# Kernel tuning notes

Hardware: AMD Instinct MI355X
Metric: run time of the kernel (lower is better)

## Reference

```python
import jax, jax.numpy as jnp
import numpy as np

WS = 7        # window_size
NH = 12       # num_heads
HD = 32       # head_dim
DIM = 384     # dim
N = WS * WS   # tokens per window


def _cpb_rel_coords():
    # log-spaced relative coords, (N, N, 2)
    c = np.stack(np.meshgrid(np.arange(WS), np.arange(WS), indexing='ij'))  # (2, ws, ws)
    cf = c.reshape(2, -1)                       # (2, N)
    rel = cf[:, :, None] - cf[:, None, :]       # (2, N, N)
    rel = rel.transpose(1, 2, 0).astype(np.float32)  # (N, N, 2)
    return np.sign(rel) * np.log1p(np.abs(rel))


def setup_inputs() -> dict:
    key = jax.random.key(0)
    ks = jax.random.split(key, 6)
    B_ = 2048
    x = jax.random.normal(ks[0], (B_, N, DIM), jnp.float32)
    mask = jnp.zeros((64, N, N), jnp.float32)  # shifted-window mask (0 / -100 pattern); zeros here
    qkv_w = jax.random.normal(ks[1], (3 * DIM, DIM), jnp.float32) * 0.02
    qkv_b = jnp.zeros((3 * DIM,), jnp.float32)
    tau = jnp.ones((NH,), jnp.float32)
    cpb_w1 = jax.random.normal(ks[2], (64, 2), jnp.float32) * 0.02
    cpb_b1 = jnp.zeros((64,), jnp.float32)
    cpb_w2 = jax.random.normal(ks[3], (NH, 64), jnp.float32) * 0.02
    cpb_b2 = jnp.zeros((NH,), jnp.float32)
    proj_w = jax.random.normal(ks[4], (DIM, DIM), jnp.float32) * 0.02
    proj_b = jnp.zeros((DIM,), jnp.float32)
    return {"x": x, "mask": mask, "qkv_w": qkv_w, "qkv_b": qkv_b, "tau": tau,
            "cpb_w1": cpb_w1, "cpb_b1": cpb_b1, "cpb_w2": cpb_w2, "cpb_b2": cpb_b2,
            "proj_w": proj_w, "proj_b": proj_b}


def reference(x, mask, qkv_w, qkv_b, tau, cpb_w1, cpb_b1, cpb_w2, cpb_b2, proj_w, proj_b):
    B_, Nt, C = x.shape
    qkv = x @ qkv_w.T + qkv_b                         # (B_, N, 3*C)
    qkv = qkv.reshape(B_, Nt, 3, NH, HD).transpose(2, 0, 3, 1, 4)  # (3, B_, H, N, hd)
    q, k, v = qkv[0], qkv[1], qkv[2]
    # cosine attention: L2-normalize q, k (F.normalize eps=1e-12)
    q = q / jnp.maximum(jnp.linalg.norm(q, axis=-1, keepdims=True), 1e-12)
    k = k / jnp.maximum(jnp.linalg.norm(k, axis=-1, keepdims=True), 1e-12)
    attn = jnp.einsum('bhnd,bhmd->bhnm', q, k)        # (B_, H, N, N)
    attn = attn / jnp.maximum(tau, 0.01)[None, :, None, None]
    # log-CPB bias
    rel = jnp.asarray(_cpb_rel_coords())              # (N, N, 2)
    cpb = jax.nn.relu(rel @ cpb_w1.T + cpb_b1) @ cpb_w2.T + cpb_b2  # (N, N, H)
    attn = attn + cpb.transpose(2, 0, 1)[None]        # broadcast over B_
    # shifted-window mask
    nW = mask.shape[0]
    B = B_ // nW
    attn = (attn.reshape(B, nW, NH, Nt, Nt) + mask[None, :, None]).reshape(B_, NH, Nt, Nt)
    attn = jax.nn.softmax(attn, axis=-1)
    y = jnp.einsum('bhnm,bhmd->bnhd', attn, v).reshape(B_, Nt, C)
    return y @ proj_w.T + proj_b
```

## Files before the change

### kernel.cpp

```cpp
#include <hip/hip_runtime.h>


typedef float f32x4 __attribute__((ext_vector_type(4)));
typedef __bf16 bf16x8 __attribute__((ext_vector_type(8)));
typedef unsigned short u16;
typedef u16 u16x8 __attribute__((ext_vector_type(8)));
typedef u16 u16x4 __attribute__((ext_vector_type(4)));
typedef unsigned u32x4 __attribute__((ext_vector_type(4)));

__device__ __forceinline__ float b2f(unsigned u) {
  return __builtin_bit_cast(float, u << 16);
}
__device__ __forceinline__ u16 f2b(float f) {
  unsigned u = __builtin_bit_cast(unsigned, f);
  u += 0x7fffu + ((u >> 16) & 1u);
  return (u16)(u >> 16);
}
__device__ __forceinline__ unsigned pack2(float a, float b) {
  return (unsigned)f2b(a) | ((unsigned)f2b(b) << 16);
}

#define GLD16(gp, lp)                                        \
  __builtin_amdgcn_global_load_lds(                          \
      (const __attribute__((address_space(1))) void*)(gp),   \
      (__attribute__((address_space(3))) void*)(lp), 16, 0, 0)

__global__ __launch_bounds__(256) void k_cast(const float* __restrict__ in,
                                              u16* __restrict__ out, int n8) {
  int i = blockIdx.x * 256 + threadIdx.x;
  if (i >= n8) return;
  const float4* p = reinterpret_cast<const float4*>(in) + (size_t)i * 2;
  float4 a = p[0], b = p[1];
  u16x8 r;
  r[0] = f2b(a.x); r[1] = f2b(a.y); r[2] = f2b(a.z); r[3] = f2b(a.w);
  r[4] = f2b(b.x); r[5] = f2b(b.y); r[6] = f2b(b.z); r[7] = f2b(b.w);
  *(reinterpret_cast<u16x8*>(out) + i) = r;
}

__global__ __launch_bounds__(64) void k_cpb(const float* __restrict__ w1,
                                            const float* __restrict__ b1,
                                            const float* __restrict__ w2,
                                            const float* __restrict__ b2,
                                            float* __restrict__ cpb_t) {
  int p = blockIdx.x * 64 + threadIdx.x;
  if (p >= 49 * 49) return;
  int n = p / 49, m = p % 49;
  float d0 = (float)(n / 7 - m / 7);
  float d1 = (float)(n % 7 - m % 7);
  float a0 = log1pf(fabsf(d0)); a0 = (d0 < 0.f) ? -a0 : a0;
  float a1 = log1pf(fabsf(d1)); a1 = (d1 < 0.f) ? -a1 : a1;
  float acc[12];
#pragma unroll
  for (int h = 0; h < 12; ++h) acc[h] = b2[h];
  for (int j = 0; j < 64; ++j) {
    float hj = fmaxf(a0 * w1[2 * j] + a1 * w1[2 * j + 1] + b1[j], 0.f);
#pragma unroll
    for (int h = 0; h < 12; ++h) acc[h] += hj * w2[h * 64 + j];
  }
#pragma unroll
  for (int h = 0; h < 12; ++h) cpb_t[h * 2401 + p] = acc[h];
}

__global__ __launch_bounds__(256) void k_comb(const float* __restrict__ cpb_t,
                                              const float* __restrict__ mask,
                                              float* __restrict__ comb) {
  const int wh = blockIdx.x;
  const int h = wh >> 6, w = wh & 63;
  const float* c = cpb_t + h * 2401;
  const float* m = mask + (size_t)w * 2401;
  float* o = comb + (size_t)wh * 2548;
  for (int p = threadIdx.x; p < 2548; p += 256) {
    int n = p / 52, mc = p % 52;
    float v = (mc < 49) ? c[n * 49 + mc] + m[n * 49 + mc] : 0.f;
    o[p] = v;
  }
}

template <bool OUT_F32>
__global__ __launch_bounds__(256) void k_gemm_bt(
    const u16* __restrict__ A, const u16* __restrict__ W,
    const float* __restrict__ bias, void* __restrict__ Cv,
    int M, int N, int K) {
  (void)M;
  __shared__ __align__(16) u16 sA[2][4096];
  __shared__ __align__(16) u16 sB[2][4096];
  const int tid = threadIdx.x;
  const int cpx = (int)(gridDim.x >> 3);
  int bid = (int)blockIdx.x;
  bid = (bid & 7) * cpx + (bid >> 3);
  const int nt = N >> 7;
  const int m0 = (bid / nt) << 7;
  const int n0 = (bid % nt) << 7;
  const int srow = tid >> 2;
  const int scs = (((tid & 3) ^ ((srow >> 1) & 3)) << 3);
  const u16* ga0 = A + (size_t)(m0 + srow) * K + scs;
  const u16* ga1 = ga0 + (size_t)64 * K;
  const u16* gw0 = W + (size_t)(n0 + srow) * K + scs;
  const u16* gw1 = gw0 + (size_t)64 * K;
  const int KT = K >> 5;

#define STAGE(buf, kk)                              \
  do {                                              \
    GLD16(ga0 + (kk), &sA[buf][tid * 8]);           \
    GLD16(ga1 + (kk), &sA[buf][2048 + tid * 8]);    \
    GLD16(gw0 + (kk), &sB[buf][tid * 8]);           \
    GLD16(gw1 + (kk), &sB[buf][2048 + tid * 8]);    \
  } while (0)

  STAGE(0, 0);

  const f32x4 z4 = {0.f, 0.f, 0.f, 0.f};
  f32x4 acc[4][4];
#pragma unroll
  for (int i = 0; i < 4; ++i)
#pragma unroll
    for (int j = 0; j < 4; ++j) acc[i][j] = z4;

  const int l = tid & 63, w = tid >> 6;
  const int wm = (w >> 1) << 6, wn = (w & 1) << 6;
  const int lr = l & 15, lg = l >> 4;
  const int arow = wm + lr, brow = wn + lr;
  const int cg = ((lg ^ ((lr >> 1) & 3)) << 3);

  for (int t = 0; t < KT; ++t) {
    __syncthreads();
    if (t + 1 < KT) STAGE((t + 1) & 1, (t + 1) * 32);
    const u16* pa = sA[t & 1];
    const u16* pb = sB[t & 1];
    bf16x8 af[4], bfv[4];
#pragma unroll
    for (int mi = 0; mi < 4; ++mi)
      af[mi] = __builtin_bit_cast(bf16x8,
          *reinterpret_cast<const u16x8*>(pa + (arow + mi * 16) * 32 + cg));
#pragma unroll
    for (int ni = 0; ni < 4; ++ni)
      bfv[ni] = __builtin_bit_cast(bf16x8,
          *reinterpret_cast<const u16x8*>(pb + (brow + ni * 16) * 32 + cg));
#pragma unroll
    for (int mi = 0; mi < 4; ++mi)
#pragma unroll
      for (int ni = 0; ni < 4; ++ni)
        acc[mi][ni] = __builtin_amdgcn_mfma_f32_16x16x32_bf16(
            af[mi], bfv[ni], acc[mi][ni], 0, 0, 0);
  }
#undef STAGE

  float bv[4];
#pragma unroll
  for (int ni = 0; ni < 4; ++ni) bv[ni] = bias[n0 + wn + ni * 16 + lr];
#pragma unroll
  for (int mi = 0; mi < 4; ++mi)
#pragma unroll
    for (int r = 0; r < 4; ++r) {
      const size_t row = (size_t)(m0 + wm + mi * 16 + lg * 4 + r);
#pragma unroll
      for (int ni = 0; ni < 4; ++ni) {
        const int col = n0 + wn + ni * 16 + lr;
        float v = acc[mi][ni][r] + bv[ni];
        if (OUT_F32)
          reinterpret_cast<float*>(Cv)[row * N + col] = v;
        else
          reinterpret_cast<u16*>(Cv)[row * N + col] = f2b(v);
      }
    }
}

__global__ __launch_bounds__(64, 4) void k_attn(
    const u16* __restrict__ qkv, const float* __restrict__ tau,
    const float* __restrict__ comb, u16* __restrict__ y) {
  const int b = blockIdx.x, h = blockIdx.y;
  const int l = threadIdx.x;
  __shared__ __align__(16) u16 lk[64][40];
  __shared__ __align__(16) u16 lq[64][40];
  u16(*vt)[72] = reinterpret_cast<u16(*)[72]>(&lk[0][0]);

  const float tauh = fmaxf(tau[h], 0.01f);
  const bool valid = l < 49;
  u16x8 v8s[4];
  {
    const u16* base = qkv + ((size_t)b * 49 + (valid ? l : 0)) * 1152 + h * 32;
    float qv[32], kv[32];
#pragma unroll
    for (int c = 0; c < 4; ++c) {
      u16x8 q8 = {0, 0, 0, 0, 0, 0, 0, 0};
      u16x8 k8 = {0, 0, 0, 0, 0, 0, 0, 0};
      u16x8 v8 = {0, 0, 0, 0, 0, 0, 0, 0};
      if (valid) {
        q8 = *reinterpret_cast<const u16x8*>(base + c * 8);
        k8 = *reinterpret_cast<const u16x8*>(base + 384 + c * 8);
        v8 = *reinterpret_cast<const u16x8*>(base + 768 + c * 8);
      }
      v8s[c] = v8;
#pragma unroll
      for (int e = 0; e < 8; ++e) {
        qv[c * 8 + e] = b2f((unsigned)q8[e]);
        kv[c * 8 + e] = b2f((unsigned)k8[e]);
      }
    }
    float sq = 0.f, sk = 0.f;
#pragma unroll
    for (int j = 0; j < 32; ++j) { sq += qv[j] * qv[j]; sk += kv[j] * kv[j]; }
    const float qs = (1.f / fmaxf(sqrtf(sq), 1e-12f)) / tauh;
    const float ks = 1.f / fmaxf(sqrtf(sk), 1e-12f);
#pragma unroll
    for (int c = 0; c < 4; ++c) {
      u16x8 wq, wk;
#pragma unroll
      for (int e = 0; e < 8; ++e) {
        wq[e] = f2b(qv[c * 8 + e] * qs);
        wk[e] = f2b(kv[c * 8 + e] * ks);
      }
      *reinterpret_cast<u16x8*>(&lq[l][c * 8]) = wq;
      *reinterpret_cast<u16x8*>(&lk[l][c * 8]) = wk;
    }
  }
  __syncthreads();

  const int lr = l & 15, lg = l >> 4;
  bf16x8 kf[4];
#pragma unroll
  for (int mi = 0; mi < 4; ++mi)
    kf[mi] = __builtin_bit_cast(bf16x8,
        *reinterpret_cast<const u16x8*>(&lk[mi * 16 + lr][lg * 8]));
  __syncthreads();
#pragma unroll
  for (int c = 0; c < 4; ++c)
#pragma unroll
    for (int e = 0; e < 8; ++e) vt[c * 8 + e][l] = v8s[c][e];
  __syncthreads();
  bf16x8 vtf[2][2];
#pragma unroll
  for (int dd = 0; dd < 2; ++dd)
#pragma unroll
    for (int ks = 0; ks < 2; ++ks)
      vtf[dd][ks] = __builtin_bit_cast(bf16x8,
          *reinterpret_cast<const u16x8*>(&vt[dd * 16 + lr][ks * 32 + lg * 8]));

  const f32x4 z4 = {0.f, 0.f, 0.f, 0.f};
  const int src0 = lr + 16 * ((2 * lg) & 3);
  const int src1 = lr + 16 * ((2 * lg + 1) & 3);
  const bool hi5 = lg >= 2;
  const float* bbase = comb + (size_t)(h * 64 + (b & 63)) * 2548;

#pragma unroll
  for (int nj = 0; nj < 4; ++nj) {
    const bf16x8 qf = __builtin_bit_cast(bf16x8,
        *reinterpret_cast<const u16x8*>(&lq[nj * 16 + lr][lg * 8]));
    f32x4 s[4];
#pragma unroll
    for (int mi = 0; mi < 4; ++mi)
      s[mi] = __builtin_amdgcn_mfma_f32_16x16x32_bf16(kf[mi], qf, z4, 0, 0, 0);

    const int n = nj * 16 + lr;
    const float* bp = bbase + (size_t)(n < 49 ? n : 48) * 52 + lg * 4;
    f32x4 bia[4];
#pragma unroll
    for (int mi = 0; mi < 4; ++mi)
      bia[mi] = *reinterpret_cast<const f32x4*>(bp + mi * 16);

    float v[4][4];
#pragma unroll
    for (int mi = 0; mi < 3; ++mi)
#pragma unroll
      for (int r = 0; r < 4; ++r) v[mi][r] = s[mi][r] + bia[mi][r];
#pragma unroll
    for (int r = 0; r < 4; ++r) {
      float t = s[3][r] + bia[3][r];
      v[3][r] = (lg == 0 && r == 0) ? t : -1e30f;
    }

    float mx = v[0][0];
#pragma unroll
    for (int mi = 0; mi < 4; ++mi)
#pragma unroll
      for (int r = 0; r < 4; ++r) mx = fmaxf(mx, v[mi][r]);
    mx = fmaxf(mx, __shfl_xor(mx, 16));
    mx = fmaxf(mx, __shfl_xor(mx, 32));
    float sum = 0.f;
#pragma unroll
    for (int mi = 0; mi < 4; ++mi)
#pragma unroll
      for (int r = 0; r < 4; ++r) {
        v[mi][r] = __expf(v[mi][r] - mx);
        sum += v[mi][r];
      }
    sum += __shfl_xor(sum, 16);
    sum += __shfl_xor(sum, 32);
    const float rinv = __builtin_amdgcn_rcpf(sum);

    unsigned pk[4][2];
#pragma unroll
    for (int mi = 0; mi < 4; ++mi) {
      pk[mi][0] = pack2(v[mi][0] * rinv, v[mi][1] * rinv);
      pk[mi][1] = pack2(v[mi][2] * rinv, v[mi][3] * rinv);
    }
    bf16x8 pf[2];
#pragma unroll
    for (int ks = 0; ks < 2; ++ks) {
      unsigned a0 = (unsigned)__shfl((int)pk[2 * ks][0], src0);
      unsigned b0 = (unsigned)__shfl((int)pk[2 * ks + 1][0], src0);
      unsigned a1 = (unsigned)__shfl((int)pk[2 * ks][1], src0);
      unsigned b1 = (unsigned)__shfl((int)pk[2 * ks + 1][1], src0);
      unsigned a2 = (unsigned)__shfl((int)pk[2 * ks][0], src1);
      unsigned b2_ = (unsigned)__shfl((int)pk[2 * ks + 1][0], src1);
      unsigned a3 = (unsigned)__shfl((int)pk[2 * ks][1], src1);
      unsigned b3 = (unsigned)__shfl((int)pk[2 * ks + 1][1], src1);
      u32x4 ww = {hi5 ? b0 : a0, hi5 ? b1 : a1, hi5 ? b2_ : a2, hi5 ? b3 : a3};
      pf[ks] = __builtin_bit_cast(bf16x8, ww);
    }

    f32x4 o0 = __builtin_amdgcn_mfma_f32_16x16x32_bf16(vtf[0][0], pf[0], z4, 0, 0, 0);
    o0 = __builtin_amdgcn_mfma_f32_16x16x32_bf16(vtf[0][1], pf[1], o0, 0, 0, 0);
    f32x4 o1 = __builtin_amdgcn_mfma_f32_16x16x32_bf16(vtf[1][0], pf[0], z4, 0, 0, 0);
    o1 = __builtin_amdgcn_mfma_f32_16x16x32_bf16(vtf[1][1], pf[1], o1, 0, 0, 0);

    if (n < 49) {
      u16* dst = y + ((size_t)b * 49 + n) * 384 + h * 32 + lg * 4;
      u16x4 w0 = {f2b(o0[0]), f2b(o0[1]), f2b(o0[2]), f2b(o0[3])};
      u16x4 w1 = {f2b(o1[0]), f2b(o1[1]), f2b(o1[2]), f2b(o1[3])};
      *reinterpret_cast<u16x4*>(dst) = w0;
      *reinterpret_cast<u16x4*>(dst + 16) = w1;
    }
  }
}

extern "C" void kernel_launch(void* const* d_in, const int* in_sizes, int n_in,
                              void* d_out, int out_size, void* d_ws,
                              size_t ws_size, hipStream_t stream) {
  (void)in_sizes; (void)n_in; (void)out_size; (void)ws_size;
  const float* x      = (const float*)d_in[0];
  const float* mask   = (const float*)d_in[1];
  const float* qkv_w  = (const float*)d_in[2];
  const float* qkv_b  = (const float*)d_in[3];
  const float* tau    = (const float*)d_in[4];
  const float* cpb_w1 = (const float*)d_in[5];
  const float* cpb_b1 = (const float*)d_in[6];
  const float* cpb_w2 = (const float*)d_in[7];
  const float* cpb_b2 = (const float*)d_in[8];
  const float* proj_w = (const float*)d_in[9];
  const float* proj_b = (const float*)d_in[10];
  float* out = (float*)d_out;

  char* ws = (char*)d_ws;
  u16* x_bf     = (u16*)(ws);
  u16* qkvw_bf  = (u16*)(ws + 77070336);
  u16* projw_bf = (u16*)(ws + 77955072);
  float* cpb_t  = (float*)(ws + 78249984);
  u16* qkv_bf   = (u16*)(ws + 78365696);
  u16* y_bf     = (u16*)(ws + 309576704);
  float* comb   = (float*)(ws + 386647040);

  k_cast<<<dim3(18816), dim3(256), 0, stream>>>(x, x_bf, 4816896);
  k_cast<<<dim3(216), dim3(256), 0, stream>>>(qkv_w, qkvw_bf, 55296);
  k_cast<<<dim3(72), dim3(256), 0, stream>>>(proj_w, projw_bf, 18432);
  k_cpb<<<dim3(38), dim3(64), 0, stream>>>(cpb_w1, cpb_b1, cpb_w2, cpb_b2, cpb_t);
  k_comb<<<dim3(768), dim3(256), 0, stream>>>(cpb_t, mask, comb);

  k_gemm_bt<false><<<dim3(784 * 9), dim3(256), 0, stream>>>(
      x_bf, qkvw_bf, qkv_b, qkv_bf, 100352, 1152, 384);

  k_attn<<<dim3(2048, 12), dim3(64), 0, stream>>>(qkv_bf, tau, comb, y_bf);

  k_gemm_bt<true><<<dim3(784 * 3), dim3(256), 0, stream>>>(
      y_bf, projw_bf, proj_b, out, 100352, 384, 384);
}
```

Measured before the change: 423.5 us.

## Rewrite GEMM as 512-thread 256x128 tile with triple-buffered K=64 pipeline

```diff
diff --git a/kernel.cpp b/kernel.cpp
--- a/kernel.cpp
+++ b/kernel.cpp
@@ -24,6 +24,13 @@
   __builtin_amdgcn_global_load_lds(                          \
       (const __attribute__((address_space(1))) void*)(gp),   \
       (__attribute__((address_space(3))) void*)(lp), 16, 0, 0)
+
+#define BARF()                            \
+  do {                                    \
+    asm volatile("" ::: "memory");        \
+    __builtin_amdgcn_s_barrier();         \
+    asm volatile("" ::: "memory");        \
+  } while (0)
 
 __global__ __launch_bounds__(256) void k_cast(const float* __restrict__ in,
                                               u16* __restrict__ out, int n8) {
@@ -77,37 +84,41 @@
 }
 
 template <bool OUT_F32>
-__global__ __launch_bounds__(256) void k_gemm_bt(
+__global__ __launch_bounds__(512, 2) void k_gemm8(
     const u16* __restrict__ A, const u16* __restrict__ W,
-    const float* __restrict__ bias, void* __restrict__ Cv,
-    int M, int N, int K) {
-  (void)M;
-  __shared__ __align__(16) u16 sA[2][4096];
-  __shared__ __align__(16) u16 sB[2][4096];
+    const float* __restrict__ bias, void* __restrict__ Cv, int N) {
+  __shared__ __align__(16) u16 sA[3][16384];
+  __shared__ __align__(16) u16 sB[3][8192];
   const int tid = threadIdx.x;
   const int cpx = (int)(gridDim.x >> 3);
   int bid = (int)blockIdx.x;
   bid = (bid & 7) * cpx + (bid >> 3);
   const int nt = N >> 7;
-  const int m0 = (bid / nt) << 7;
+  const int m0 = (bid / nt) << 8;
   const int n0 = (bid % nt) << 7;
-  const int srow = tid >> 2;
-  const int scs = (((tid & 3) ^ ((srow >> 1) & 3)) << 3);
-  const u16* ga0 = A + (size_t)(m0 + srow) * K + scs;
-  const u16* ga1 = ga0 + (size_t)64 * K;
-  const u16* gw0 = W + (size_t)(n0 + srow) * K + scs;
-  const u16* gw1 = gw0 + (size_t)64 * K;
-  const int KT = K >> 5;
-
-#define STAGE(buf, kk)                              \
-  do {                                              \
-    GLD16(ga0 + (kk), &sA[buf][tid * 8]);           \
-    GLD16(ga1 + (kk), &sA[buf][2048 + tid * 8]);    \
-    GLD16(gw0 + (kk), &sB[buf][tid * 8]);           \
-    GLD16(gw1 + (kk), &sB[buf][2048 + tid * 8]);    \
-  } while (0)
-
-  STAGE(0, 0);
+
+  const int r0 = tid >> 3;
+  const int g = (((tid & 7) ^ (r0 & 7)) << 3);
+  const u16* pAg = A + (size_t)(m0 + r0) * 384 + g;
+  const u16* pBg = W + (size_t)(n0 + r0) * 384 + g;
+
+#define GA(buf, t, i) GLD16(pAg + (i) * 24576 + (t) * 64, &sA[buf][(i) * 4096 + tid * 8])
+#define GB(buf, t, i) GLD16(pBg + (i) * 24576 + (t) * 64, &sB[buf][(i) * 4096 + tid * 8])
+
+  GA(0, 0, 0); GA(0, 0, 1); GA(0, 0, 2); GA(0, 0, 3); GB(0, 0, 0); GB(0, 0, 1);
+  GA(1, 1, 0); GA(1, 1, 1); GA(1, 1, 2); GA(1, 1, 3); GB(1, 1, 0); GB(1, 1, 1);
+
+  const int l = tid & 63, w = tid >> 6;
+  const int wm = (w & 3) << 6, wn = (w >> 2) << 6;
+  const int lr = l & 15, lg = l >> 4;
+  const int ax = lr & 7;
+  const int sl0 = ((lg ^ ax) << 3), sl1 = (((4 | lg) ^ ax) << 3);
+  int aOff[4], bOff[4];
+#pragma unroll
+  for (int i = 0; i < 4; ++i) {
+    aOff[i] = (wm + i * 16 + lr) << 6;
+    bOff[i] = (wn + i * 16 + lr) << 6;
+  }
 
   const f32x4 z4 = {0.f, 0.f, 0.f, 0.f};
   f32x4 acc[4][4];
@@ -116,34 +127,61 @@
 #pragma unroll
     for (int j = 0; j < 4; ++j) acc[i][j] = z4;
 
-  const int l = tid & 63, w = tid >> 6;
-  const int wm = (w >> 1) << 6, wn = (w & 1) << 6;
-  const int lr = l & 15, lg = l >> 4;
-  const int arow = wm + lr, brow = wn + lr;
-  const int cg = ((lg ^ ((lr >> 1) & 3)) << 3);
-
-  for (int t = 0; t < KT; ++t) {
-    __syncthreads();
-    if (t + 1 < KT) STAGE((t + 1) & 1, (t + 1) * 32);
-    const u16* pa = sA[t & 1];
-    const u16* pb = sB[t & 1];
-    bf16x8 af[4], bfv[4];
+  asm volatile("s_waitcnt vmcnt(6)" ::: "memory");
+  __builtin_amdgcn_s_barrier();
+
+#pragma unroll
+  for (int t = 0; t < 6; ++t) {
+    const u16* pa = sA[t % 3];
+    const u16* pb = sB[t % 3];
+    const int nb = (t + 2) % 3;
+    bf16x8 af[4], bq[4];
 #pragma unroll
     for (int mi = 0; mi < 4; ++mi)
       af[mi] = __builtin_bit_cast(bf16x8,
-          *reinterpret_cast<const u16x8*>(pa + (arow + mi * 16) * 32 + cg));
+          *reinterpret_cast<const u16x8*>(pa + aOff[mi] + sl0));
 #pragma unroll
     for (int ni = 0; ni < 4; ++ni)
-      bfv[ni] = __builtin_bit_cast(bf16x8,
-          *reinterpret_cast<const u16x8*>(pb + (brow + ni * 16) * 32 + cg));
+      bq[ni] = __builtin_bit_cast(bf16x8,
+          *reinterpret_cast<const u16x8*>(pb + bOff[ni] + sl0));
+    if (t < 4) { GA(nb, t + 2, 0); GA(nb, t + 2, 1); GA(nb, t + 2, 2); }
+    BARF();
+    __builtin_amdgcn_s_setprio(1);
 #pragma unroll
     for (int mi = 0; mi < 4; ++mi)
 #pragma unroll
       for (int ni = 0; ni < 4; ++ni)
         acc[mi][ni] = __builtin_amdgcn_mfma_f32_16x16x32_bf16(
-            af[mi], bfv[ni], acc[mi][ni], 0, 0, 0);
-  }
-#undef STAGE
+            af[mi], bq[ni], acc[mi][ni], 0, 0, 0);
+    __builtin_amdgcn_s_setprio(0);
+    BARF();
+#pragma unroll
+    for (int mi = 0; mi < 4; ++mi)
+      af[mi] = __builtin_bit_cast(bf16x8,
+          *reinterpret_cast<const u16x8*>(pa + aOff[mi] + sl1));
+#pragma unroll
+    for (int ni = 0; ni < 4; ++ni)
+      bq[ni] = __builtin_bit_cast(bf16x8,
+          *reinterpret_cast<const u16x8*>(pb + bOff[ni] + sl1));
+    if (t < 4) { GA(nb, t + 2, 3); GB(nb, t + 2, 0); GB(nb, t + 2, 1); }
+    BARF();
+    __builtin_amdgcn_s_setprio(1);
+#pragma unroll
+    for (int mi = 0; mi < 4; ++mi)
+#pragma unroll
+      for (int ni = 0; ni < 4; ++ni)
+        acc[mi][ni] = __builtin_amdgcn_mfma_f32_16x16x32_bf16(
+            af[mi], bq[ni], acc[mi][ni], 0, 0, 0);
+    __builtin_amdgcn_s_setprio(0);
+    if (t < 4) {
+      asm volatile("s_waitcnt vmcnt(6)" ::: "memory");
+    } else if (t == 4) {
+      asm volatile("s_waitcnt vmcnt(0)" ::: "memory");
+    }
+    BARF();
+  }
+#undef GA
+#undef GB
 
   float bv[4];
 #pragma unroll
@@ -151,12 +189,12 @@
 #pragma unroll
   for (int mi = 0; mi < 4; ++mi)
 #pragma unroll
-    for (int r = 0; r < 4; ++r) {
-      const size_t row = (size_t)(m0 + wm + mi * 16 + lg * 4 + r);
+    for (int rr = 0; rr < 4; ++rr) {
+      const size_t row = (size_t)(m0 + wm + mi * 16 + lg * 4 + rr);
 #pragma unroll
       for (int ni = 0; ni < 4; ++ni) {
         const int col = n0 + wn + ni * 16 + lr;
-        float v = acc[mi][ni][r] + bv[ni];
+        float v = acc[mi][ni][rr] + bv[ni];
         if (OUT_F32)
           reinterpret_cast<float*>(Cv)[row * N + col] = v;
         else
@@ -356,11 +394,11 @@
   k_cpb<<<dim3(38), dim3(64), 0, stream>>>(cpb_w1, cpb_b1, cpb_w2, cpb_b2, cpb_t);
   k_comb<<<dim3(768), dim3(256), 0, stream>>>(cpb_t, mask, comb);
 
-  k_gemm_bt<false><<<dim3(784 * 9), dim3(256), 0, stream>>>(
-      x_bf, qkvw_bf, qkv_b, qkv_bf, 100352, 1152, 384);
+  k_gemm8<false><<<dim3(392 * 9), dim3(512), 0, stream>>>(
+      x_bf, qkvw_bf, qkv_b, qkv_bf, 1152);
 
   k_attn<<<dim3(2048, 12), dim3(64), 0, stream>>>(qkv_bf, tau, comb, y_bf);
 
-  k_gemm_bt<true><<<dim3(784 * 3), dim3(256), 0, stream>>>(
-      y_bf, projw_bf, proj_b, out, 100352, 384, 384);
-}
+  k_gemm8<true><<<dim3(392 * 3), dim3(512), 0, stream>>>(
+      y_bf, projw_bf, proj_b, out, 384);
+}
```

New measurement: 450.8 us. +6.4%, slower.

## Add 256x256-tile 4-stage pipelined QKV GEMM with N padded to 1280

Applied to the files above, without the earlier changes.

```diff
diff --git a/kernel.cpp b/kernel.cpp
--- a/kernel.cpp
+++ b/kernel.cpp
@@ -24,6 +24,13 @@
   __builtin_amdgcn_global_load_lds(                          \
       (const __attribute__((address_space(1))) void*)(gp),   \
       (__attribute__((address_space(3))) void*)(lp), 16, 0, 0)
+
+#define BARF()                            \
+  do {                                    \
+    asm volatile("" ::: "memory");        \
+    __builtin_amdgcn_s_barrier();         \
+    asm volatile("" ::: "memory");        \
+  } while (0)
 
 __global__ __launch_bounds__(256) void k_cast(const float* __restrict__ in,
                                               u16* __restrict__ out, int n8) {
@@ -74,6 +81,121 @@
     float v = (mc < 49) ? c[n * 49 + mc] + m[n * 49 + mc] : 0.f;
     o[p] = v;
   }
+}
+
+__global__ __launch_bounds__(512, 2) void k_gemmQ(
+    const u16* __restrict__ A, const u16* __restrict__ W,
+    const float* __restrict__ bias, u16* __restrict__ C) {
+  __shared__ __align__(16) u16 sA[4][8192];
+  __shared__ __align__(16) u16 sB[4][8192];
+  const int tid = threadIdx.x;
+  const int cpx = (int)(gridDim.x >> 3);
+  int bid = (int)blockIdx.x;
+  bid = (bid & 7) * cpx + (bid >> 3);
+  const int m0 = (bid / 5) << 8;
+  const int n0 = (bid % 5) << 8;
+
+  const int r0 = tid >> 2;
+  const int gc = (((tid & 3) ^ ((r0 >> 1) & 3)) << 3);
+  const u16* pA = A + (size_t)(m0 + r0) * 384 + gc;
+  const u16* pB = W + (size_t)(n0 + r0) * 384 + gc;
+
+#define QA(buf, t, i) GLD16(pA + (size_t)(i)*49152 + (t)*32, &sA[buf][(i)*4096 + tid * 8])
+#define QB(buf, t, i) GLD16(pB + (size_t)(i)*49152 + (t)*32, &sB[buf][(i)*4096 + tid * 8])
+
+  QA(0, 0, 0); QA(0, 0, 1); QB(0, 0, 0); QB(0, 0, 1);
+  QA(1, 1, 0); QA(1, 1, 1); QB(1, 1, 0); QB(1, 1, 1);
+  QA(2, 2, 0); QA(2, 2, 1); QB(2, 2, 0); QB(2, 2, 1);
+
+  const int l = tid & 63, w = tid >> 6;
+  const int wr = w >> 2, wc = w & 3;
+  const int lr = l & 15, lg = l >> 4;
+  const int sl = ((lg ^ ((lr >> 1) & 3)) << 3);
+  int aOff[8], bOff[4];
+#pragma unroll
+  for (int i = 0; i < 8; ++i) aOff[i] = ((wr * 128 + i * 16 + lr) << 5) + sl;
+#pragma unroll
+  for (int i = 0; i < 4; ++i) bOff[i] = ((wc * 64 + i * 16 + lr) << 5) + sl;
+
+  const f32x4 z4 = {0.f, 0.f, 0.f, 0.f};
+  f32x4 acc[8][4];
+#pragma unroll
+  for (int i = 0; i < 8; ++i)
+#pragma unroll
+    for (int j = 0; j < 4; ++j) acc[i][j] = z4;
+
+  asm volatile("s_waitcnt vmcnt(8)" ::: "memory");
+  __builtin_amdgcn_s_barrier();
+
+#pragma unroll
+  for (int t = 0; t < 12; ++t) {
+    const u16* pa = sA[t & 3];
+    const u16* pb = sB[t & 3];
+    const int nb = (t + 3) & 3;
+    bf16x8 af[4], bq[4];
+#pragma unroll
+    for (int i = 0; i < 4; ++i)
+      af[i] = __builtin_bit_cast(bf16x8,
+          *reinterpret_cast<const u16x8*>(pa + aOff[i]));
+#pragma unroll
+    for (int i = 0; i < 4; ++i)
+      bq[i] = __builtin_bit_cast(bf16x8,
+          *reinterpret_cast<const u16x8*>(pb + bOff[i]));
+    if (t < 9) { QA(nb, t + 3, 0); QA(nb, t + 3, 1); }
+    BARF();
+    __builtin_amdgcn_s_setprio(1);
+#pragma unroll
+    for (int fa = 0; fa < 4; ++fa)
+#pragma unroll
+      for (int fb = 0; fb < 4; ++fb)
+        acc[fa][fb] = __builtin_amdgcn_mfma_f32_16x16x32_bf16(
+            af[fa], bq[fb], acc[fa][fb], 0, 0, 0);
+    __builtin_amdgcn_s_setprio(0);
+    BARF();
+#pragma unroll
+    for (int i = 0; i < 4; ++i)
+      af[i] = __builtin_bit_cast(bf16x8,
+          *reinterpret_cast<const u16x8*>(pa + aOff[4 + i]));
+#pragma unroll
+    for (int i = 0; i < 4; ++i)
+      bq[i] = __builtin_bit_cast(bf16x8,
+          *reinterpret_cast<const u16x8*>(pb + bOff[i]));
+    if (t < 9) { QB(nb, t + 3, 0); QB(nb, t + 3, 1); }
+    BARF();
+    __builtin_amdgcn_s_setprio(1);
+#pragma unroll
+    for (int fa = 0; fa < 4; ++fa)
+#pragma unroll
+      for (int fb = 0; fb < 4; ++fb)
+        acc[4 + fa][fb] = __builtin_amdgcn_mfma_f32_16x16x32_bf16(
+            af[fa], bq[fb], acc[4 + fa][fb], 0, 0, 0);
+    __builtin_amdgcn_s_setprio(0);
+    if (t <= 8) {
+      asm volatile("s_waitcnt vmcnt(8)" ::: "memory");
+    } else if (t == 9) {
+      asm volatile("s_waitcnt vmcnt(4)" ::: "memory");
+    } else if (t == 10) {
+      asm volatile("s_waitcnt vmcnt(0)" ::: "memory");
+    }
+    BARF();
+  }
+#undef QA
+#undef QB
+
+  float bv[4];
+#pragma unroll
+  for (int fb = 0; fb < 4; ++fb) bv[fb] = bias[n0 + wc * 64 + fb * 16 + lr];
+#pragma unroll
+  for (int fa = 0; fa < 8; ++fa)
+#pragma unroll
+    for (int rr = 0; rr < 4; ++rr) {
+      const size_t row = (size_t)(m0 + wr * 128 + fa * 16 + lg * 4 + rr);
+#pragma unroll
+      for (int fb = 0; fb < 4; ++fb) {
+        const int col = n0 + wc * 64 + fb * 16 + lr;
+        C[row * 1280 + col] = f2b(acc[fa][fb][rr] + bv[fb]);
+      }
+    }
 }
 
 template <bool OUT_F32>
@@ -178,7 +300,7 @@
   const bool valid = l < 49;
   u16x8 v8s[4];
   {
-    const u16* base = qkv + ((size_t)b * 49 + (valid ? l : 0)) * 1152 + h * 32;
+    const u16* base = qkv + ((size_t)b * 49 + (valid ? l : 0)) * 1280 + h * 32;
     float qv[32], kv[32];
 #pragma unroll
     for (int c = 0; c < 4; ++c) {
@@ -343,12 +465,17 @@
 
   char* ws = (char*)d_ws;
   u16* x_bf     = (u16*)(ws);
+  u16* y_bf     = (u16*)(ws);
   u16* qkvw_bf  = (u16*)(ws + 77070336);
-  u16* projw_bf = (u16*)(ws + 77955072);
-  float* cpb_t  = (float*)(ws + 78249984);
-  u16* qkv_bf   = (u16*)(ws + 78365696);
-  u16* y_bf     = (u16*)(ws + 309576704);
-  float* comb   = (float*)(ws + 386647040);
+  u16* projw_bf = (u16*)(ws + 78053376);
+  float* cpb_t  = (float*)(ws + 78348288);
+  float* qkvb_p = (float*)(ws + 78464000);
+  u16* qkv_bf   = (u16*)(ws + 78469120);
+  float* comb   = (float*)(ws + 335370240);
+
+  hipMemsetAsync(qkvw_bf + 1152 * 384, 0, (1280 - 1152) * 384 * 2, stream);
+  hipMemsetAsync(qkvb_p, 0, 1280 * 4, stream);
+  hipMemcpyAsync(qkvb_p, qkv_b, 1152 * 4, hipMemcpyDeviceToDevice, stream);
 
   k_cast<<<dim3(18816), dim3(256), 0, stream>>>(x, x_bf, 4816896);
   k_cast<<<dim3(216), dim3(256), 0, stream>>>(qkv_w, qkvw_bf, 55296);
@@ -356,8 +483,7 @@
   k_cpb<<<dim3(38), dim3(64), 0, stream>>>(cpb_w1, cpb_b1, cpb_w2, cpb_b2, cpb_t);
   k_comb<<<dim3(768), dim3(256), 0, stream>>>(cpb_t, mask, comb);
 
-  k_gemm_bt<false><<<dim3(784 * 9), dim3(256), 0, stream>>>(
-      x_bf, qkvw_bf, qkv_b, qkv_bf, 100352, 1152, 384);
+  k_gemmQ<<<dim3(392 * 5), dim3(512), 0, stream>>>(x_bf, qkvw_bf, qkvb_p, qkv_bf);
 
   k_attn<<<dim3(2048, 12), dim3(64), 0, stream>>>(qkv_bf, tau, comb, y_bf);
 
```

After: 443.8 us. 4.8% more time.

## Use 128-thread GEMM blocks with 64x128 per-wave tiles and fixed K

Applied to the files above, without the earlier changes.

```diff
diff --git a/kernel.cpp b/kernel.cpp
--- a/kernel.cpp
+++ b/kernel.cpp
@@ -77,11 +77,9 @@
 }
 
 template <bool OUT_F32>
-__global__ __launch_bounds__(256) void k_gemm_bt(
+__global__ __launch_bounds__(128, 2) void k_gemm(
     const u16* __restrict__ A, const u16* __restrict__ W,
-    const float* __restrict__ bias, void* __restrict__ Cv,
-    int M, int N, int K) {
-  (void)M;
+    const float* __restrict__ bias, void* __restrict__ Cv, int N) {
   __shared__ __align__(16) u16 sA[2][4096];
   __shared__ __align__(16) u16 sB[2][4096];
   const int tid = threadIdx.x;
@@ -91,72 +89,78 @@
   const int nt = N >> 7;
   const int m0 = (bid / nt) << 7;
   const int n0 = (bid % nt) << 7;
-  const int srow = tid >> 2;
-  const int scs = (((tid & 3) ^ ((srow >> 1) & 3)) << 3);
-  const u16* ga0 = A + (size_t)(m0 + srow) * K + scs;
-  const u16* ga1 = ga0 + (size_t)64 * K;
-  const u16* gw0 = W + (size_t)(n0 + srow) * K + scs;
-  const u16* gw1 = gw0 + (size_t)64 * K;
-  const int KT = K >> 5;
-
-#define STAGE(buf, kk)                              \
-  do {                                              \
-    GLD16(ga0 + (kk), &sA[buf][tid * 8]);           \
-    GLD16(ga1 + (kk), &sA[buf][2048 + tid * 8]);    \
-    GLD16(gw0 + (kk), &sB[buf][tid * 8]);           \
-    GLD16(gw1 + (kk), &sB[buf][2048 + tid * 8]);    \
+
+  const int r0 = tid >> 2;
+  const int gc = (((tid & 3) ^ ((r0 >> 1) & 3)) << 3);
+  const u16* gA = A + (size_t)(m0 + r0) * 384 + gc;
+  const u16* gB = W + (size_t)(n0 + r0) * 384 + gc;
+
+#define STAGE(buf, kk)                                  \
+  do {                                                  \
+    GLD16(gA + (kk), &sA[buf][tid * 8]);                \
+    GLD16(gA + 12288 + (kk), &sA[buf][1024 + tid * 8]); \
+    GLD16(gA + 24576 + (kk), &sA[buf][2048 + tid * 8]); \
+    GLD16(gA + 36864 + (kk), &sA[buf][3072 + tid * 8]); \
+    GLD16(gB + (kk), &sB[buf][tid * 8]);                \
+    GLD16(gB + 12288 + (kk), &sB[buf][1024 + tid * 8]); \
+    GLD16(gB + 24576 + (kk), &sB[buf][2048 + tid * 8]); \
+    GLD16(gB + 36864 + (kk), &sB[buf][3072 + tid * 8]); \
   } while (0)
 
   STAGE(0, 0);
 
+  const int l = tid & 63, w = tid >> 6;
+  const int lr = l & 15, lg = l >> 4;
+  const int sl = ((lg ^ ((lr >> 1) & 3)) << 3);
+  int aOff[4], bOff[8];
+#pragma unroll
+  for (int i = 0; i < 4; ++i) aOff[i] = ((w * 64 + i * 16 + lr) << 5) + sl;
+#pragma unroll
+  for (int j = 0; j < 8; ++j) bOff[j] = ((j * 16 + lr) << 5) + sl;
+
   const f32x4 z4 = {0.f, 0.f, 0.f, 0.f};
-  f32x4 acc[4][4];
+  f32x4 acc[4][8];
 #pragma unroll
   for (int i = 0; i < 4; ++i)
 #pragma unroll
-    for (int j = 0; j < 4; ++j) acc[i][j] = z4;
-
-  const int l = tid & 63, w = tid >> 6;
-  const int wm = (w >> 1) << 6, wn = (w & 1) << 6;
-  const int lr = l & 15, lg = l >> 4;
-  const int arow = wm + lr, brow = wn + lr;
-  const int cg = ((lg ^ ((lr >> 1) & 3)) << 3);
-
-  for (int t = 0; t < KT; ++t) {
+    for (int j = 0; j < 8; ++j) acc[i][j] = z4;
+
+#pragma unroll 4
+  for (int t = 0; t < 12; ++t) {
     __syncthreads();
-    if (t + 1 < KT) STAGE((t + 1) & 1, (t + 1) * 32);
+    if (t + 1 < 12) STAGE((t + 1) & 1, (t + 1) * 32);
     const u16* pa = sA[t & 1];
     const u16* pb = sB[t & 1];
-    bf16x8 af[4], bfv[4];
-#pragma unroll
-    for (int mi = 0; mi < 4; ++mi)
-      af[mi] = __builtin_bit_cast(bf16x8,
-          *reinterpret_cast<const u16x8*>(pa + (arow + mi * 16) * 32 + cg));
-#pragma unroll
-    for (int ni = 0; ni < 4; ++ni)
-      bfv[ni] = __builtin_bit_cast(bf16x8,
-          *reinterpret_cast<const u16x8*>(pb + (brow + ni * 16) * 32 + cg));
-#pragma unroll
-    for (int mi = 0; mi < 4; ++mi)
-#pragma unroll
-      for (int ni = 0; ni < 4; ++ni)
-        acc[mi][ni] = __builtin_amdgcn_mfma_f32_16x16x32_bf16(
-            af[mi], bfv[ni], acc[mi][ni], 0, 0, 0);
+    bf16x8 af[4], bq[8];
+#pragma unroll
+    for (int i = 0; i < 4; ++i)
+      af[i] = __builtin_bit_cast(bf16x8,
+          *reinterpret_cast<const u16x8*>(pa + aOff[i]));
+#pragma unroll
+    for (int j = 0; j < 8; ++j)
+      bq[j] = __builtin_bit_cast(bf16x8,
+          *reinterpret_cast<const u16x8*>(pb + bOff[j]));
+#pragma unroll
+    for (int i = 0; i < 4; ++i)
+#pragma unroll
+      for (int j = 0; j < 8; ++j)
+        acc[i][j] = __builtin_amdgcn_mfma_f32_16x16x32_bf16(
+            af[i], bq[j], acc[i][j], 0, 0, 0);
   }
 #undef STAGE
 
-  float bv[4];
-#pragma unroll
-  for (int ni = 0; ni < 4; ++ni) bv[ni] = bias[n0 + wn + ni * 16 + lr];
-#pragma unroll
-  for (int mi = 0; mi < 4; ++mi)
-#pragma unroll
-    for (int r = 0; r < 4; ++r) {
-      const size_t row = (size_t)(m0 + wm + mi * 16 + lg * 4 + r);
-#pragma unroll
-      for (int ni = 0; ni < 4; ++ni) {
-        const int col = n0 + wn + ni * 16 + lr;
-        float v = acc[mi][ni][r] + bv[ni];
+  float bv[8];
+#pragma unroll
+  for (int j = 0; j < 8; ++j) bv[j] = bias[n0 + j * 16 + lr];
+#pragma unroll
+  for (int i = 0; i < 4; ++i)
+#pragma unroll
+    for (int rr = 0; rr < 4; ++rr) {
+      const size_t row = (size_t)(m0 + w * 64 + i * 16 + lg * 4 + rr);
+#pragma unroll
+      for (int j = 0; j < 8; ++j) {
+        const int col = n0 + j * 16 + lr;
+        float v = acc[i][j][rr] + bv[j];
         if (OUT_F32)
           reinterpret_cast<float*>(Cv)[row * N + col] = v;
         else
@@ -356,11 +360,11 @@
   k_cpb<<<dim3(38), dim3(64), 0, stream>>>(cpb_w1, cpb_b1, cpb_w2, cpb_b2, cpb_t);
   k_comb<<<dim3(768), dim3(256), 0, stream>>>(cpb_t, mask, comb);
 
-  k_gemm_bt<false><<<dim3(784 * 9), dim3(256), 0, stream>>>(
-      x_bf, qkvw_bf, qkv_b, qkv_bf, 100352, 1152, 384);
+  k_gemm<false><<<dim3(784 * 9), dim3(128), 0, stream>>>(
+      x_bf, qkvw_bf, qkv_b, qkv_bf, 1152);
 
   k_attn<<<dim3(2048, 12), dim3(64), 0, stream>>>(qkv_bf, tau, comb, y_bf);
 
-  k_gemm_bt<true><<<dim3(784 * 3), dim3(256), 0, stream>>>(
-      y_bf, projw_bf, proj_b, out, 100352, 384, 384);
-}
+  k_gemm<true><<<dim3(784 * 3), dim3(128), 0, stream>>>(
+      y_bf, projw_bf, proj_b, out, 384);
+}
```

Result: no change. 425.3 us (+0.4%).
